# Kernel optimization log

Measured on AMD Instinct MI355X. Metric: run time of the kernel, lower is better.

Reference implementation:

```python
import jax, jax.numpy as jnp
import numpy as np

D_MODEL = 768
N_HEADS = 12

def setup_inputs() -> dict:
    key = jax.random.key(0)
    ks = jax.random.split(key, 5)
    D = D_MODEL
    x = jax.random.normal(ks[0], (2, 4096, D), dtype=jnp.float32)
    s_attn = 1.0 / np.sqrt(D)
    s_proj = 1.0 / np.sqrt(D)
    W_attn = jax.random.uniform(ks[1], (D, 3 * D), minval=-s_attn, maxval=s_attn, dtype=jnp.float32)
    b_attn = jax.random.uniform(ks[2], (3 * D,), minval=-s_attn, maxval=s_attn, dtype=jnp.float32)
    W_proj = jax.random.uniform(ks[3], (D, D), minval=-s_proj, maxval=s_proj, dtype=jnp.float32)
    b_proj = jax.random.uniform(ks[4], (D,), minval=-s_proj, maxval=s_proj, dtype=jnp.float32)
    return {"x": x, "W_attn": W_attn, "b_attn": b_attn, "W_proj": W_proj, "b_proj": b_proj}

def reference(x, W_attn, b_attn, W_proj, b_proj):
    B, T, C = x.shape
    H = N_HEADS
    hd = C // H
    qkv = x @ W_attn + b_attn                     # [B,T,3C]
    q, k, v = jnp.split(qkv, 3, axis=-1)
    # [B,T,C] -> [B,H,T,hd]
    q = q.reshape(B, T, H, hd).transpose(0, 2, 1, 3)
    k = k.reshape(B, T, H, hd).transpose(0, 2, 1, 3)
    v = v.reshape(B, T, H, hd).transpose(0, 2, 1, 3)
    att = jnp.einsum('bhqd,bhkd->bhqk', q, k) * (1.0 / np.sqrt(hd))
    causal = jnp.tril(jnp.ones((T, T), dtype=bool))
    att = jnp.where(causal, att, -jnp.inf)
    att = jax.nn.softmax(att, axis=-1)
    y = jnp.einsum('bhqk,bhkd->bhqd', att, v)     # [B,H,T,hd]
    y = y.transpose(0, 2, 1, 3).reshape(B, T, C)
    return y @ W_proj + b_proj
```

## Files before the change

kernel.cpp:

```cpp
#include <hip/hip_runtime.h>
#include <hip/hip_bf16.h>

typedef __attribute__((ext_vector_type(8))) short bf16x8;
typedef __attribute__((ext_vector_type(4))) float f32x4;
typedef __attribute__((ext_vector_type(16))) float f32x16;
typedef __attribute__((ext_vector_type(4))) int i32x4;

#define DEVI __device__ __forceinline__

namespace {
constexpr int BATCH = 2;
constexpr int T = 4096;
constexpr int C = 768;
constexpr int H = 12;
constexpr int HD = 64;
constexpr int M = BATCH * T;
constexpr int N3 = 3 * C;
constexpr int BH = BATCH * H;
constexpr float QSCALE = 0.125f * 1.44269504088896f;
}

DEVI ushort f2b(float f) {
  union { float f; unsigned u; } v; v.f = f;
  unsigned r = (v.u + 0x7FFFu + ((v.u >> 16) & 1u)) >> 16;
  return (ushort)r;
}

DEVI f32x16 zero16() {
  f32x16 z;
#pragma unroll
  for (int i = 0; i < 16; i++) z[i] = 0.f;
  return z;
}

DEVI void gload16(const void* g, void* l) {
  __builtin_amdgcn_global_load_lds(
      (const __attribute__((address_space(1))) unsigned int*)g,
      (__attribute__((address_space(3))) unsigned int*)l, 16, 0, 0);
}

__global__ __launch_bounds__(256) void cvt_kernel(const float* __restrict__ src,
                                                  ushort* __restrict__ dst, int n) {
  int i = (blockIdx.x * 256 + threadIdx.x) * 4;
  int stride = gridDim.x * 256 * 4;
  for (; i < n; i += stride) {
    float4 v = *reinterpret_cast<const float4*>(src + i);
    ushort4 o;
    o.x = f2b(v.x); o.y = f2b(v.y); o.z = f2b(v.z); o.w = f2b(v.w);
    *reinterpret_cast<ushort4*>(dst + i) = o;
  }
}

__global__ __launch_bounds__(256) void cvtT_kernel(const float* __restrict__ src,
                                                   ushort* __restrict__ dst,
                                                   int K, int N) {
  __shared__ ushort Lt[64 * 68];
  const int k0 = blockIdx.x * 64, n0 = blockIdx.y * 64;
  const int tid = threadIdx.x;
  const int rr = tid >> 4, c4 = (tid & 15) * 4;
#pragma unroll
  for (int it = 0; it < 4; it++) {
    const int r = it * 16 + rr;
    float4 v = *reinterpret_cast<const float4*>(src + (size_t)(k0 + r) * N + n0 + c4);
    Lt[(c4 + 0) * 68 + r] = f2b(v.x);
    Lt[(c4 + 1) * 68 + r] = f2b(v.y);
    Lt[(c4 + 2) * 68 + r] = f2b(v.z);
    Lt[(c4 + 3) * 68 + r] = f2b(v.w);
  }
  __syncthreads();
#pragma unroll
  for (int it = 0; it < 4; it++) {
    const int r = it * 16 + rr;
    *reinterpret_cast<ushort4*>(dst + (size_t)(n0 + r) * K + k0 + c4) =
        *reinterpret_cast<const ushort4*>(&Lt[r * 68 + c4]);
  }
}

template <int EPI>
__global__ __launch_bounds__(256, 3) void gemm_kernel(
    const ushort* __restrict__ A, const ushort* __restrict__ Bt,
    const float* __restrict__ bias, int N, int Kd,
    ushort* __restrict__ qo, ushort* __restrict__ ko, ushort* __restrict__ vo,
    float* __restrict__ fo) {
  constexpr int BM = (EPI == 0) ? 128 : 64;
  constexpr int BN = 128;
  constexpr int WN = (EPI == 0) ? 2 : 4;
  constexpr int WTN = BN / WN;
  constexpr int NT = WTN / 32;
  constexpr int CH_A = BM / 8;
  constexpr int CH_B = BN / 8;
  constexpr int CPW = (CH_A + CH_B) / 4;
  constexpr int SMEM = (EPI == 0) ? (4 * 64 * 68) : ((BM + BN) * 64);
  __shared__ ushort smem[SMEM];
  ushort* As = smem;
  ushort* Bs = smem + BM * 64;

  const int tid = threadIdx.x;
  const int lane = tid & 63;
  const int w = tid >> 6;
  const int l31 = lane & 31;
  const int hi = lane >> 5;
  const int wm = w / WN, wn = w % WN;
  const int m0 = blockIdx.y * BM, n0 = blockIdx.x * BN;
  const int r8 = lane >> 3, c8 = lane & 7;
  const int csw = (c8 ^ r8) * 8;

  f32x16 acc[2][NT];
#pragma unroll
  for (int mt = 0; mt < 2; mt++)
#pragma unroll
    for (int nt = 0; nt < NT; nt++) acc[mt][nt] = zero16();

  for (int k0 = 0; k0 < Kd; k0 += 64) {
    __syncthreads();
#pragma unroll
    for (int ci = 0; ci < CPW; ci++) {
      const int chk = w * CPW + ci;
      if (chk < CH_A) {
        gload16(A + (size_t)(m0 + chk * 8 + r8) * Kd + k0 + csw, (char*)As + chk * 1024);
      } else {
        const int ch2 = chk - CH_A;
        gload16(Bt + (size_t)(n0 + ch2 * 8 + r8) * Kd + k0 + csw, (char*)Bs + ch2 * 1024);
      }
    }
    __syncthreads();
#pragma unroll
    for (int ks = 0; ks < 4; ks++) {
      bf16x8 af[2], bf[NT];
#pragma unroll
      for (int mt = 0; mt < 2; mt++) {
        const int rl = wm * 64 + mt * 32 + l31;
        af[mt] = *reinterpret_cast<const bf16x8*>(
            &As[rl * 64 + ((ks * 16 + hi * 8) ^ ((rl & 7) * 8))]);
      }
#pragma unroll
      for (int nt = 0; nt < NT; nt++) {
        const int nl = wn * WTN + nt * 32 + l31;
        bf[nt] = *reinterpret_cast<const bf16x8*>(
            &Bs[nl * 64 + ((ks * 16 + hi * 8) ^ ((nl & 7) * 8))]);
      }
#pragma unroll
      for (int mt = 0; mt < 2; mt++)
#pragma unroll
        for (int nt = 0; nt < NT; nt++)
          acc[mt][nt] = __builtin_amdgcn_mfma_f32_32x32x16_bf16(af[mt], bf[nt], acc[mt][nt], 0, 0, 0);
    }
  }

  if constexpr (EPI == 0) {
    if (n0 >= 1536) {
      __syncthreads();
      ushort* Vw = smem + w * 4352;
      const float bv0 = bias[n0 + wn * 64 + l31];
      const float bv1 = bias[n0 + wn * 64 + 32 + l31];
#pragma unroll
      for (int mt = 0; mt < 2; mt++)
#pragma unroll
        for (int nt = 0; nt < 2; nt++) {
          const float bv = nt ? bv1 : bv0;
#pragma unroll
          for (int r = 0; r < 16; r++) {
            const int trow = mt * 32 + (r & 3) + ((r >> 2) << 3) + (hi << 2);
            Vw[(nt * 32 + l31) * 68 + trow] = f2b(acc[mt][nt][r] + bv);
          }
        }
      const int hh = (n0 - 1536) / 64 + wn;
      const int bb = m0 >> 12;
      const int t0 = (m0 & (T - 1)) + wm * 64;
      const size_t vbase = (size_t)((bb * H + hh) * 64 + lane) * T + t0;
#pragma unroll
      for (int x8 = 0; x8 < 8; x8++) {
        bf16x8 vv = *reinterpret_cast<const bf16x8*>(&Vw[lane * 68 + x8 * 8]);
        *reinterpret_cast<bf16x8*>(vo + vbase + ((x8 ^ (lane & 7)) * 8)) = vv;
      }
    } else {
#pragma unroll
      for (int mt = 0; mt < 2; mt++)
#pragma unroll
        for (int nt = 0; nt < 2; nt++) {
          const int n = n0 + wn * 64 + nt * 32 + l31;
          const float bv = bias[n];
          const int part = (n >= 768) ? 1 : 0;
          const int ci = n - part * 768;
          const int hh = ci >> 6, dd = ci & 63;
#pragma unroll
          for (int r = 0; r < 16; r++) {
            const int m = m0 + wm * 64 + mt * 32 + (r & 3) + ((r >> 2) << 3) + (hi << 2);
            const int bb = m >> 12, t = m & (T - 1);
            const float val = acc[mt][nt][r] + bv;
            if (part == 0) {
              qo[((size_t)(bb * H + hh) * T + t) * HD + dd] = f2b(val * QSCALE);
            } else {
              ko[((size_t)(bb * H + hh) * T + t) * HD + (dd ^ ((t & 7) << 3))] = f2b(val);
            }
          }
        }
    }
  } else {
#pragma unroll
    for (int mt = 0; mt < 2; mt++)
#pragma unroll
      for (int nt = 0; nt < NT; nt++) {
        const int n = n0 + wn * WTN + nt * 32 + l31;
        const float bv = bias[n];
#pragma unroll
        for (int r = 0; r < 16; r++) {
          const int m = m0 + wm * 64 + mt * 32 + (r & 3) + ((r >> 2) << 3) + (hi << 2);
          fo[(size_t)m * N + n] = acc[mt][nt][r] + bv;
        }
      }
  }
}

__global__ __launch_bounds__(128, 2) void attn_kernel(
    const ushort* __restrict__ Qg, const ushort* __restrict__ Kg,
    const ushort* __restrict__ Vtg, ushort* __restrict__ Yg) {
  __shared__ ushort smem[16384 + 2 * 32 * 36];

  const int tid = threadIdx.x;
  const int lane = tid & 63;
  const int w = tid >> 6;
  const int l31 = lane & 31;
  const int hi = lane >> 5;
  const int r8 = lane >> 3, c8 = lane & 7;

  const int bid = blockIdx.x;
  const int xcd = bid & 7, idx = bid >> 3;
  const int bh = xcd * 3 + idx % 3;
  const int a = idx / 3;

  const int bb = bh / H, h = bh % H;
  const ushort* Qp = Qg + (size_t)bh * T * HD;
  const char* Kbp = (const char*)(Kg + (size_t)bh * T * HD);
  const char* Vbp = (const char*)(Vtg + (size_t)bh * HD * T);

  bf16x8 qfa[4], qfb[4], qcur[4];
  const int qr0 = a * 64 + w * 32 + l31;
  const int qr1 = (63 - a) * 64 + w * 32 + l31;
#pragma unroll
  for (int ks = 0; ks < 4; ks++) {
    qfa[ks] = *reinterpret_cast<const bf16x8*>(Qp + (size_t)qr0 * HD + ks * 16 + hi * 8);
    qfb[ks] = *reinterpret_cast<const bf16x8*>(Qp + (size_t)qr1 * HD + ks * 16 + hi * 8);
    qcur[ks] = qfa[ks];
  }

  int q0 = a * 64;
  int q0w = q0 + w * 32;
  int qc = q0w + l31;

  float mrun = -1e30f, lrun = 0.f;
  f32x16 o16[2];
  o16[0] = zero16();
  o16[1] = zero16();

  const int boundary = a + 1;
  const int nt_tot = 65;

  auto kv0_of = [&](int tt) { return (tt < boundary ? tt : tt - boundary) * 64; };

  auto issue_tile = [&](int tt) {
    const int kv0 = kv0_of(tt);
    ushort* kb = smem + (tt & 1) * 8192;
    ushort* vb = kb + 4096;
#pragma unroll
    for (int c2 = 0; c2 < 4; c2++) {
      const int chk = w * 4 + c2;
      gload16(Kbp + ((size_t)(kv0 + chk * 8 + r8) * 64 + c8 * 8) * 2, (char*)kb + chk * 1024);
      gload16(Vbp + ((size_t)(chk * 8 + r8) * T + kv0 + c8 * 8) * 2, (char*)vb + chk * 1024);
    }
  };

  auto epilogue = [&](int q0p, float lr) {
    ushort* Yt = smem + 16384 + w * 1152;
    const float linv = 1.0f / lr;
#pragma unroll
    for (int dt = 0; dt < 2; dt++) {
#pragma unroll
      for (int r = 0; r < 16; r++) {
        const int d32 = (r & 3) + ((r >> 2) << 3) + (hi << 2);
        Yt[l31 * 36 + d32] = f2b(o16[dt][r] * linv);
      }
#pragma unroll
      for (int seg = 0; seg < 2; seg++) {
        bf16x8 vv = *reinterpret_cast<const bf16x8*>(&Yt[l31 * 36 + hi * 16 + seg * 8]);
        *reinterpret_cast<bf16x8*>(
            Yg + ((size_t)(bb * T + q0p + w * 32 + l31)) * C + h * 64 + dt * 32 + hi * 16 + seg * 8) = vv;
      }
    }
  };

  issue_tile(0);

  for (int tt = 0; tt < nt_tot; tt++) {
    if (tt + 1 < nt_tot) {
      issue_tile(tt + 1);
      asm volatile("s_waitcnt vmcnt(8)" ::: "memory");
    } else {
      asm volatile("s_waitcnt vmcnt(0)" ::: "memory");
    }
    __builtin_amdgcn_s_barrier();
    __builtin_amdgcn_sched_barrier(0);

    if (tt == boundary) {
      epilogue(q0, lrun);
      mrun = -1e30f; lrun = 0.f;
      o16[0] = zero16(); o16[1] = zero16();
#pragma unroll
      for (int ks = 0; ks < 4; ks++) qcur[ks] = qfb[ks];
      q0 = (63 - a) * 64;
      q0w = q0 + w * 32;
      qc = q0w + l31;
    }

    const int kv0 = kv0_of(tt);
    const ushort* Ks = smem + (tt & 1) * 8192;
    const ushort* Vs = Ks + 4096;

    const bool have[2] = {kv0 <= q0w + 31, kv0 + 32 <= q0w + 31};
    const bool needm[2] = {kv0 + 31 > q0w, kv0 + 63 > q0w};

    f32x16 s2[2];
    s2[0] = zero16();
    s2[1] = zero16();
    __builtin_amdgcn_s_setprio(1);
#pragma unroll
    for (int sub = 0; sub < 2; sub++) {
      if (!have[sub]) continue;
      const int row = sub * 32 + l31;
      const int sw = (row & 7) << 3;
#pragma unroll
      for (int ks = 0; ks < 4; ks++) {
        bf16x8 kf = *reinterpret_cast<const bf16x8*>(&Ks[row * 64 + ((ks * 16 + hi * 8) ^ sw)]);
        s2[sub] = __builtin_amdgcn_mfma_f32_32x32x16_bf16(kf, qcur[ks], s2[sub], 0, 0, 0);
      }
      if (needm[sub]) {
#pragma unroll
        for (int r2 = 0; r2 < 16; r2++) {
          const int kv = kv0 + sub * 32 + (r2 & 3) + ((r2 >> 2) << 3) + (hi << 2);
          if (kv > qc) s2[sub][r2] = -1e30f;
        }
      }
    }
    __builtin_amdgcn_s_setprio(0);

    float pa = -1e30f, pb = -1e30f, pc = -1e30f, pd = -1e30f;
#pragma unroll
    for (int sub = 0; sub < 2; sub++) {
      if (!have[sub]) continue;
#pragma unroll
      for (int r2 = 0; r2 < 16; r2 += 4) {
        pa = fmaxf(pa, s2[sub][r2]);
        pb = fmaxf(pb, s2[sub][r2 + 1]);
        pc = fmaxf(pc, s2[sub][r2 + 2]);
        pd = fmaxf(pd, s2[sub][r2 + 3]);
      }
    }
    float pm = fmaxf(fmaxf(pa, pb), fmaxf(pc, pd));
    pm = fmaxf(pm, __shfl_xor(pm, 32));
    if (__any(pm > mrun + 8.f)) {
      const float mnew = fmaxf(mrun, pm);
      const float corr = __builtin_amdgcn_exp2f(mrun - mnew);
      lrun *= corr;
#pragma unroll
      for (int dt = 0; dt < 2; dt++)
#pragma unroll
        for (int r2 = 0; r2 < 16; r2++) o16[dt][r2] *= corr;
      mrun = mnew;
    }
    float sa = 0.f, sb = 0.f, sc = 0.f, sd = 0.f;
#pragma unroll
    for (int sub = 0; sub < 2; sub++) {
      if (!have[sub]) continue;
#pragma unroll
      for (int r2 = 0; r2 < 16; r2 += 4) {
        s2[sub][r2]     = __builtin_amdgcn_exp2f(s2[sub][r2] - mrun);     sa += s2[sub][r2];
        s2[sub][r2 + 1] = __builtin_amdgcn_exp2f(s2[sub][r2 + 1] - mrun); sb += s2[sub][r2 + 1];
        s2[sub][r2 + 2] = __builtin_amdgcn_exp2f(s2[sub][r2 + 2] - mrun); sc += s2[sub][r2 + 2];
        s2[sub][r2 + 3] = __builtin_amdgcn_exp2f(s2[sub][r2 + 3] - mrun); sd += s2[sub][r2 + 3];
      }
    }
    float sum = (sa + sb) + (sc + sd);
    sum += __shfl_xor(sum, 32);
    lrun += sum;

#pragma unroll
    for (int sub = 0; sub < 2; sub++) {
      if (!have[sub]) continue;
#pragma unroll
      for (int ks2 = 0; ks2 < 2; ks2++) {
        const int r0 = ks2 * 8;
        int a0, a1, b0, b1;
        asm("v_cvt_pk_bf16_f32 %0, %1, %2" : "=v"(a0) : "v"(s2[sub][r0 + 0]), "v"(s2[sub][r0 + 1]));
        asm("v_cvt_pk_bf16_f32 %0, %1, %2" : "=v"(a1) : "v"(s2[sub][r0 + 2]), "v"(s2[sub][r0 + 3]));
        asm("v_cvt_pk_bf16_f32 %0, %1, %2" : "=v"(b0) : "v"(s2[sub][r0 + 4]), "v"(s2[sub][r0 + 5]));
        asm("v_cvt_pk_bf16_f32 %0, %1, %2" : "=v"(b1) : "v"(s2[sub][r0 + 6]), "v"(s2[sub][r0 + 7]));
        asm("v_permlane32_swap_b32 %0, %1" : "+v"(a0), "+v"(b0));
        asm("v_permlane32_swap_b32 %0, %1" : "+v"(a1), "+v"(b1));
        const i32x4 pi = {a0, a1, b0, b1};
        const bf16x8 pf = __builtin_bit_cast(bf16x8, pi);
        __builtin_amdgcn_s_setprio(1);
#pragma unroll
        for (int dt = 0; dt < 2; dt++) {
          const int drow = dt * 32 + l31;
          const int sw = (drow & 7) << 3;
          bf16x8 vf = *reinterpret_cast<const bf16x8*>(
              &Vs[drow * 64 + ((sub * 32 + ks2 * 16 + hi * 8) ^ sw)]);
          o16[dt] = __builtin_amdgcn_mfma_f32_32x32x16_bf16(vf, pf, o16[dt], 0, 0, 0);
        }
        __builtin_amdgcn_s_setprio(0);
      }
    }

    asm volatile("s_waitcnt lgkmcnt(0)" ::: "memory");
    __builtin_amdgcn_s_barrier();
  }

  epilogue(q0, lrun);
}

extern "C" void kernel_launch(void* const* d_in, const int* in_sizes, int n_in,
                              void* d_out, int out_size, void* d_ws, size_t ws_size,
                              hipStream_t stream) {
  const float* x = (const float*)d_in[0];
  const float* Wa = (const float*)d_in[1];
  const float* ba = (const float*)d_in[2];
  const float* Wp = (const float*)d_in[3];
  const float* bp = (const float*)d_in[4];
  float* out = (float*)d_out;

  char* ws = (char*)d_ws;
  size_t off = 0;
  auto carve = [&](size_t bytes) {
    void* p = ws + off;
    off += (bytes + 255) & ~(size_t)255;
    return p;
  };
  ushort* xb   = (ushort*)carve((size_t)M * C * 2);
  ushort* WaT  = (ushort*)carve((size_t)N3 * C * 2);
  ushort* WpT  = (ushort*)carve((size_t)C * C * 2);
  ushort* Qb   = (ushort*)carve((size_t)BH * T * HD * 2);
  ushort* Kb   = (ushort*)carve((size_t)BH * T * HD * 2);
  ushort* Vtb  = (ushort*)carve((size_t)BH * HD * T * 2);
  ushort* Yb   = (ushort*)carve((size_t)M * C * 2);

  cvt_kernel<<<2048, 256, 0, stream>>>(x, xb, M * C);
  cvtT_kernel<<<dim3(C / 64, N3 / 64), 256, 0, stream>>>(Wa, WaT, C, N3);
  cvtT_kernel<<<dim3(C / 64, C / 64), 256, 0, stream>>>(Wp, WpT, C, C);

  gemm_kernel<0><<<dim3(N3 / 128, M / 128), 256, 0, stream>>>(
      xb, WaT, ba, N3, C, Qb, Kb, Vtb, nullptr);

  attn_kernel<<<dim3(768), 128, 0, stream>>>(Qb, Kb, Vtb, Yb);

  gemm_kernel<1><<<dim3(C / 128, M / 64), 256, 0, stream>>>(
      Yb, WpT, bp, C, C, nullptr, nullptr, nullptr, out);
}
```

Baseline: 197.1 us.

## Split causal attention KV range across blocks with partial-result combine kernel

Doubles the attention grid by splitting the KV range for the upper half of query tiles into two partial blocks. Each partial block writes unnormalized O, l and m to a workspace, and a new combine kernel merges them. The K/V double buffer becomes single buffers with staggered K-then-V prefetch, which cuts LDS use so occupancy can rise to 3 blocks per SIMD set. The cost is an extra kernel launch, global traffic for the fp32 partials, and more barriers per tile.

```diff
diff --git a/kernel.cpp b/kernel.cpp
--- a/kernel.cpp
+++ b/kernel.cpp
@@ -18,6 +18,7 @@
 constexpr int N3 = 3 * C;
 constexpr int BH = BATCH * H;
 constexpr float QSCALE = 0.125f * 1.44269504088896f;
+constexpr int PSZ = 64 * 64 + 128;
 }
 
 DEVI ushort f2b(float f) {
@@ -212,10 +213,13 @@
   }
 }
 
-__global__ __launch_bounds__(128, 2) void attn_kernel(
+__global__ __launch_bounds__(128, 3) void attn_kernel(
     const ushort* __restrict__ Qg, const ushort* __restrict__ Kg,
-    const ushort* __restrict__ Vtg, ushort* __restrict__ Yg) {
-  __shared__ ushort smem[16384 + 2 * 32 * 36];
+    const ushort* __restrict__ Vtg, ushort* __restrict__ Yg,
+    float* __restrict__ Pp) {
+  __shared__ ushort kbuf[4096];
+  __shared__ ushort vbuf[4096];
+  __shared__ ushort Yt[2 * 32 * 36];
 
   const int tid = threadIdx.x;
   const int lane = tid & 63;
@@ -225,9 +229,20 @@
   const int r8 = lane >> 3, c8 = lane & 7;
 
   const int bid = blockIdx.x;
-  const int xcd = bid & 7, idx = bid >> 3;
-  const int bh = xcd * 3 + idx % 3;
-  const int a = idx / 3;
+  const int xcd = bid & 7;
+  const int bh = xcd * 3 + (bid >> 3) % 3;
+  const int slot = (bid >> 3) / 3;
+
+  int qtA, qtB, kvbase, bnd, ntot;
+  bool partial;
+  if (slot < 16) {
+    qtA = slot; qtB = 31 - slot; kvbase = 0; bnd = slot + 1; ntot = 33; partial = false;
+  } else if (slot < 48) {
+    qtA = slot + 16; qtB = -1; kvbase = 0; bnd = 32; ntot = 32; partial = true;
+  } else {
+    const int a = slot - 48;
+    qtA = 32 + a; qtB = 63 - a; kvbase = 32; bnd = a + 1; ntot = 33; partial = true;
+  }
 
   const int bb = bh / H, h = bh % H;
   const ushort* Qp = Qg + (size_t)bh * T * HD;
@@ -235,87 +250,103 @@
   const char* Vbp = (const char*)(Vtg + (size_t)bh * HD * T);
 
   bf16x8 qfa[4], qfb[4], qcur[4];
-  const int qr0 = a * 64 + w * 32 + l31;
-  const int qr1 = (63 - a) * 64 + w * 32 + l31;
 #pragma unroll
   for (int ks = 0; ks < 4; ks++) {
-    qfa[ks] = *reinterpret_cast<const bf16x8*>(Qp + (size_t)qr0 * HD + ks * 16 + hi * 8);
-    qfb[ks] = *reinterpret_cast<const bf16x8*>(Qp + (size_t)qr1 * HD + ks * 16 + hi * 8);
+    qfa[ks] = *reinterpret_cast<const bf16x8*>(
+        Qp + (size_t)(qtA * 64 + w * 32 + l31) * HD + ks * 16 + hi * 8);
     qcur[ks] = qfa[ks];
   }
-
-  int q0 = a * 64;
+  if (qtB >= 0) {
+#pragma unroll
+    for (int ks = 0; ks < 4; ks++)
+      qfb[ks] = *reinterpret_cast<const bf16x8*>(
+          Qp + (size_t)(qtB * 64 + w * 32 + l31) * HD + ks * 16 + hi * 8);
+  }
+
+  int q0 = qtA * 64;
   int q0w = q0 + w * 32;
   int qc = q0w + l31;
+  float* Pcur = partial ? (Pp + (size_t)((bh * 32 + (qtA - 32)) * 2 + (slot >= 48 ? 1 : 0)) * PSZ)
+                        : nullptr;
 
   float mrun = -1e30f, lrun = 0.f;
   f32x16 o16[2];
   o16[0] = zero16();
   o16[1] = zero16();
 
-  const int boundary = a + 1;
-  const int nt_tot = 65;
-
-  auto kv0_of = [&](int tt) { return (tt < boundary ? tt : tt - boundary) * 64; };
-
-  auto issue_tile = [&](int tt) {
-    const int kv0 = kv0_of(tt);
-    ushort* kb = smem + (tt & 1) * 8192;
-    ushort* vb = kb + 4096;
+  auto kvt_of = [&](int tt) { return kvbase + (tt < bnd ? tt : tt - bnd); };
+
+  auto issue_K = [&](int tt) {
+    const int kv0 = kvt_of(tt) * 64;
 #pragma unroll
     for (int c2 = 0; c2 < 4; c2++) {
       const int chk = w * 4 + c2;
-      gload16(Kbp + ((size_t)(kv0 + chk * 8 + r8) * 64 + c8 * 8) * 2, (char*)kb + chk * 1024);
-      gload16(Vbp + ((size_t)(chk * 8 + r8) * T + kv0 + c8 * 8) * 2, (char*)vb + chk * 1024);
+      gload16(Kbp + ((size_t)(kv0 + chk * 8 + r8) * 64 + c8 * 8) * 2, (char*)kbuf + chk * 1024);
     }
   };
+  auto issue_V = [&](int tt) {
+    const int kv0 = kvt_of(tt) * 64;
+#pragma unroll
+    for (int c2 = 0; c2 < 4; c2++) {
+      const int chk = w * 4 + c2;
+      gload16(Vbp + ((size_t)(chk * 8 + r8) * T + kv0 + c8 * 8) * 2, (char*)vbuf + chk * 1024);
+    }
+  };
 
   auto epilogue = [&](int q0p, float lr) {
-    ushort* Yt = smem + 16384 + w * 1152;
+    ushort* Yw = Yt + w * 1152;
     const float linv = 1.0f / lr;
 #pragma unroll
     for (int dt = 0; dt < 2; dt++) {
 #pragma unroll
       for (int r = 0; r < 16; r++) {
         const int d32 = (r & 3) + ((r >> 2) << 3) + (hi << 2);
-        Yt[l31 * 36 + d32] = f2b(o16[dt][r] * linv);
+        Yw[l31 * 36 + d32] = f2b(o16[dt][r] * linv);
       }
 #pragma unroll
       for (int seg = 0; seg < 2; seg++) {
-        bf16x8 vv = *reinterpret_cast<const bf16x8*>(&Yt[l31 * 36 + hi * 16 + seg * 8]);
+        bf16x8 vv = *reinterpret_cast<const bf16x8*>(&Yw[l31 * 36 + hi * 16 + seg * 8]);
         *reinterpret_cast<bf16x8*>(
             Yg + ((size_t)(bb * T + q0p + w * 32 + l31)) * C + h * 64 + dt * 32 + hi * 16 + seg * 8) = vv;
       }
     }
   };
 
-  issue_tile(0);
-
-  for (int tt = 0; tt < nt_tot; tt++) {
-    if (tt + 1 < nt_tot) {
-      issue_tile(tt + 1);
-      asm volatile("s_waitcnt vmcnt(8)" ::: "memory");
-    } else {
-      asm volatile("s_waitcnt vmcnt(0)" ::: "memory");
-    }
+  auto pwrite = [&](float* P, float lr, float mr) {
+#pragma unroll
+    for (int dt = 0; dt < 2; dt++)
+#pragma unroll
+      for (int r = 0; r < 16; r++) {
+        const int d = dt * 32 + (r & 3) + ((r >> 2) << 3) + (hi << 2);
+        P[d * 64 + w * 32 + l31] = o16[dt][r];
+      }
+    P[4096 + w * 32 + l31] = lr;
+    P[4160 + w * 32 + l31] = mr;
+  };
+
+  issue_K(0);
+
+  for (int tt = 0; tt < ntot; tt++) {
+    asm volatile("s_waitcnt vmcnt(0)" ::: "memory");
     __builtin_amdgcn_s_barrier();
     __builtin_amdgcn_sched_barrier(0);
 
-    if (tt == boundary) {
-      epilogue(q0, lrun);
+    if (tt == bnd) {
+      if (partial) pwrite(Pcur, lrun, mrun);
+      else epilogue(q0, lrun);
       mrun = -1e30f; lrun = 0.f;
       o16[0] = zero16(); o16[1] = zero16();
 #pragma unroll
       for (int ks = 0; ks < 4; ks++) qcur[ks] = qfb[ks];
-      q0 = (63 - a) * 64;
+      q0 = qtB * 64;
       q0w = q0 + w * 32;
       qc = q0w + l31;
-    }
-
-    const int kv0 = kv0_of(tt);
-    const ushort* Ks = smem + (tt & 1) * 8192;
-    const ushort* Vs = Ks + 4096;
-
+      if (partial) Pcur = Pp + (size_t)((bh * 32 + (qtB - 32)) * 2 + 1) * PSZ;
+    }
+
+    issue_V(tt);
+
+    const int kv0 = kvt_of(tt) * 64;
     const bool have[2] = {kv0 <= q0w + 31, kv0 + 32 <= q0w + 31};
     const bool needm[2] = {kv0 + 31 > q0w, kv0 + 63 > q0w};
 
@@ -330,7 +361,8 @@
       const int sw = (row & 7) << 3;
 #pragma unroll
       for (int ks = 0; ks < 4; ks++) {
-        bf16x8 kf = *reinterpret_cast<const bf16x8*>(&Ks[row * 64 + ((ks * 16 + hi * 8) ^ sw)]);
+        bf16x8 kf = *reinterpret_cast<const bf16x8*>(
+            &kbuf[row * 64 + ((ks * 16 + hi * 8) ^ sw)]);
         s2[sub] = __builtin_amdgcn_mfma_f32_32x32x16_bf16(kf, qcur[ks], s2[sub], 0, 0, 0);
       }
       if (needm[sub]) {
@@ -342,6 +374,11 @@
       }
     }
     __builtin_amdgcn_s_setprio(0);
+
+    asm volatile("s_waitcnt lgkmcnt(0)" ::: "memory");
+    __builtin_amdgcn_s_barrier();
+    __builtin_amdgcn_sched_barrier(0);
+    if (tt + 1 < ntot) issue_K(tt + 1);
 
     float pa = -1e30f, pb = -1e30f, pc = -1e30f, pd = -1e30f;
 #pragma unroll
@@ -382,6 +419,14 @@
     float sum = (sa + sb) + (sc + sd);
     sum += __shfl_xor(sum, 32);
     lrun += sum;
+
+    if (tt + 1 < ntot) {
+      asm volatile("s_waitcnt vmcnt(4)" ::: "memory");
+    } else {
+      asm volatile("s_waitcnt vmcnt(0)" ::: "memory");
+    }
+    __builtin_amdgcn_s_barrier();
+    __builtin_amdgcn_sched_barrier(0);
 
 #pragma unroll
     for (int sub = 0; sub < 2; sub++) {
@@ -404,18 +449,46 @@
           const int drow = dt * 32 + l31;
           const int sw = (drow & 7) << 3;
           bf16x8 vf = *reinterpret_cast<const bf16x8*>(
-              &Vs[drow * 64 + ((sub * 32 + ks2 * 16 + hi * 8) ^ sw)]);
+              &vbuf[drow * 64 + ((sub * 32 + ks2 * 16 + hi * 8) ^ sw)]);
           o16[dt] = __builtin_amdgcn_mfma_f32_32x32x16_bf16(vf, pf, o16[dt], 0, 0, 0);
         }
         __builtin_amdgcn_s_setprio(0);
       }
     }
-
-    asm volatile("s_waitcnt lgkmcnt(0)" ::: "memory");
-    __builtin_amdgcn_s_barrier();
-  }
-
-  epilogue(q0, lrun);
+  }
+
+  if (partial) pwrite(Pcur, lrun, mrun);
+  else epilogue(q0, lrun);
+}
+
+__global__ __launch_bounds__(64) void combine_kernel(const float* __restrict__ Pp,
+                                                     ushort* __restrict__ Yg) {
+  __shared__ ushort Yt[64 * 68];
+  const int bid = blockIdx.x;
+  const int bh = bid >> 5, qq = bid & 31;
+  const int bb = bh / H, h = bh % H;
+  const int q0 = (32 + qq) * 64;
+  const int q = threadIdx.x;
+  const float* P1 = Pp + (size_t)((bh * 32 + qq) * 2 + 0) * PSZ;
+  const float* P2 = Pp + (size_t)((bh * 32 + qq) * 2 + 1) * PSZ;
+  const float l1 = P1[4096 + q], m1 = P1[4160 + q];
+  const float l2 = P2[4096 + q], m2 = P2[4160 + q];
+  const float Mx = fmaxf(m1, m2);
+  const float w1 = __builtin_amdgcn_exp2f(m1 - Mx);
+  const float w2 = __builtin_amdgcn_exp2f(m2 - Mx);
+  const float inv = 1.0f / (l1 * w1 + l2 * w2);
+#pragma unroll 8
+  for (int d = 0; d < 64; d++) {
+    const float o = P1[d * 64 + q] * w1 + P2[d * 64 + q] * w2;
+    Yt[q * 68 + d] = f2b(o * inv);
+  }
+  __syncthreads();
+#pragma unroll
+  for (int seg = 0; seg < 8; seg++) {
+    bf16x8 vv = *reinterpret_cast<const bf16x8*>(&Yt[q * 68 + seg * 8]);
+    *reinterpret_cast<bf16x8*>(
+        Yg + ((size_t)(bb * T + q0 + q)) * C + h * 64 + seg * 8) = vv;
+  }
 }
 
 extern "C" void kernel_launch(void* const* d_in, const int* in_sizes, int n_in,
@@ -442,6 +515,7 @@
   ushort* Kb   = (ushort*)carve((size_t)BH * T * HD * 2);
   ushort* Vtb  = (ushort*)carve((size_t)BH * HD * T * 2);
   ushort* Yb   = (ushort*)carve((size_t)M * C * 2);
+  float*  Pp   = (float*)carve((size_t)BH * 32 * 2 * PSZ * 4);
 
   cvt_kernel<<<2048, 256, 0, stream>>>(x, xb, M * C);
   cvtT_kernel<<<dim3(C / 64, N3 / 64), 256, 0, stream>>>(Wa, WaT, C, N3);
@@ -450,7 +524,8 @@
   gemm_kernel<0><<<dim3(N3 / 128, M / 128), 256, 0, stream>>>(
       xb, WaT, ba, N3, C, Qb, Kb, Vtb, nullptr);
 
-  attn_kernel<<<dim3(768), 128, 0, stream>>>(Qb, Kb, Vtb, Yb);
+  attn_kernel<<<dim3(1536), 128, 0, stream>>>(Qb, Kb, Vtb, Yb, Pp);
+  combine_kernel<<<dim3(BH * 32), 64, 0, stream>>>(Pp, Yb);
 
   gemm_kernel<1><<<dim3(C / 128, M / 64), 256, 0, stream>>>(
       Yb, WpT, bp, C, C, nullptr, nullptr, nullptr, out);
```

After: 178.6 us. 9.4% less time.
